# Kernel optimization log

Hardware: AMD Instinct MI355X
Metric: run time of the kernel (lower is better)

The kernel has to match this reference:

```python
import jax, jax.numpy as jnp
import numpy as np

N = 10000        # nodes
E = 320000       # edges (avg degree 32)
IN = 739         # in_channels
C = 64           # hid_channels
H = 1            # heads
D = C // H       # per-head dim
L = 10           # layer_num
G = 64           # num graphs in batch
LAMBD = 1.0


def setup_inputs() -> dict:
    key = jax.random.key(0)
    ks = jax.random.split(key, 14)
    s = 0.05
    return {
        "x": jax.random.normal(ks[0], (N, IN), jnp.float32),
        "edge_index": jax.random.randint(ks[1], (2, E), 0, N, dtype=jnp.int32),
        "batch": jnp.sort(jax.random.randint(ks[2], (N,), 0, G, dtype=jnp.int32)),
        # InitFeat: Linear(739->64), ELU, Linear(64->64) (dropout = identity at eval)
        "w0": jax.random.normal(ks[3], (IN, C), jnp.float32) * s,
        "b0": jax.random.normal(ks[4], (C,), jnp.float32) * s,
        "w1": jax.random.normal(ks[5], (C, C), jnp.float32) * s,
        "b1": jax.random.normal(ks[6], (C,), jnp.float32) * s,
        # AeroConv attention vectors for k = 1..L-1
        "conv_att": jax.random.normal(ks[7], (L - 1, H, D), jnp.float32) * s,
        # UpdateZ k=0 (g = h, width D) and k=1..L-1 (g = [h, z_scale], width 2D)
        "hop_att0": jax.random.normal(ks[8], (H, D), jnp.float32) * s,
        "hop_bias0": jax.random.normal(ks[9], (H,), jnp.float32) * s,
        "hop_att": jax.random.normal(ks[10], (L - 1, H, 2 * D), jnp.float32) * s,
        "hop_bias": jax.random.normal(ks[11], (L - 1, H), jnp.float32) * s,
        # readout head Linear(64->1)
        "w_head": jax.random.normal(ks[12], (C, 1), jnp.float32) * s,
        "b_head": jax.random.normal(ks[13], (1,), jnp.float32) * s,
    }


def reference(x, edge_index, batch, w0, b0, w1, b1, conv_att,
              hop_att0, hop_bias0, hop_att, hop_bias, w_head, b_head):
    src, dst = edge_index[0], edge_index[1]

    # ---- InitFeat (dropout is identity at inference) ----
    h = x @ w0 + b0
    h = jax.nn.elu(h) @ w1 + b1              # [N, C]
    x = h

    # ---- UpdateZ, k = 0: z = h * hop_attention ----
    hh = x.reshape(N, H, D)
    attn = jnp.sum(hop_att0 * jax.nn.elu(hh), axis=-1) + hop_bias0   # [N, H]
    z = hh * attn[..., None]                 # [N, H, D]

    for i in range(L - 1):
        k = i + 1
        scale = jnp.float32(np.log(LAMBD / k + 1.0 + 1e-6))
        z_scale = z * scale                  # [N, H, D]

        # per-edge attention: elu(z_i + z_j), dot with att, softplus
        a = jax.nn.elu(z_scale[src] + z_scale[dst])                   # [E, H, D]
        a = jax.nn.softplus(jnp.sum(conv_att[i] * a, axis=-1)) + 1e-6  # [E, H]

        # symmetric normalization by scatter-summed degree
        adj_sum = jax.ops.segment_sum(a, dst, num_segments=N)         # [N, H]
        inv = jnp.maximum(adj_sum, 1e-32) ** -0.5
        na = (inv[src] * a * inv[dst])[..., None]                     # [E, H, 1]

        # weighted scatter-sum of source features
        msgs = x[src].reshape(E, H, D) * na                           # [E, H, D]
        x = jax.ops.segment_sum(msgs, dst, num_segments=N).reshape(N, C)

        # UpdateZ (k >= 1): g = [h, z_scale]
        hh = x.reshape(N, H, D)
        g = jnp.concatenate([hh, z_scale], axis=-1)                   # [N, H, 2D]
        attn = jnp.sum(hop_att[i] * jax.nn.elu(g), axis=-1) + hop_bias[i]
        z = z + hh * attn[..., None]

    # ---- readout: elu, global mean pool over batch, linear head ----
    zf = jax.nn.elu(z.reshape(N, C))
    seg_sum = jax.ops.segment_sum(zf, batch, num_segments=G)          # [G, C]
    cnt = jax.ops.segment_sum(jnp.ones((N,), zf.dtype), batch, num_segments=G)
    pooled = seg_sum / jnp.maximum(cnt, 1.0)[:, None]
    return pooled @ w_head + b_head                                   # [G, 1]
```

## Files before the change

### kernel.cpp

```cpp
#include <hip/hip_runtime.h>
#include <hip/hip_bf16.h>
#include <math.h>

#define NN     10000
#define EE     320000
#define IN_CH  739
#define CC     64
#define GG     64
#define NLAYER 9
#define NBUCK  157
#define CHUNK  2048

typedef _Float16 half_t;
typedef _Float16 h4 __attribute__((ext_vector_type(4)));

__device__ __forceinline__ float eluf(float x) {
    return x > 0.f ? x : __expf(x) - 1.f;
}
__device__ __forceinline__ float softplusf(float x) {
    return fmaxf(x, 0.f) + __logf(1.f + __expf(-fabsf(x)));
}
__device__ __forceinline__ float wave_sum(float v) {
#pragma unroll
    for (int off = 32; off > 0; off >>= 1) v += __shfl_xor(v, off, 64);
    return v;
}
__device__ __forceinline__ float4 ldh4(const half_t* p) {
    const h4 v = *(const h4*)p;
    return make_float4((float)v.x, (float)v.y, (float)v.z, (float)v.w);
}

__global__ __launch_bounds__(256) void k_gemm1_part(
    const float* __restrict__ x, const float* __restrict__ w0,
    float* __restrict__ hpart)
{
    __shared__ float xs[64 * 68];
    __shared__ float ws[64 * 64];
    const int tid = threadIdx.x;
    const int cg = tid & 15;
    const int rg = tid >> 4;
    const int split = blockIdx.x & 3;
    const int R0 = (blockIdx.x >> 2) * 64;
    const int K0 = split * 192;

    const int sk = tid & 63;
    const int sr = tid >> 6;

    float xr[16], wr[16];
    float acc[4][4] = {};

#pragma unroll
    for (int i = 0; i < 16; ++i) {
        const int r = sr + 4 * i;
        const int gr = R0 + r;
        const int gk = K0 + sk;
        xr[i] = (gr < NN && gk < IN_CH) ? x[(size_t)gr * IN_CH + gk] : 0.f;
        const int wk = K0 + r;
        wr[i] = (wk < IN_CH) ? w0[wk * CC + sk] : 0.f;
    }

    for (int t = 0; t < 3; ++t) {
        __syncthreads();
#pragma unroll
        for (int i = 0; i < 16; ++i) {
            const int r = sr + 4 * i;
            xs[r * 68 + sk] = xr[i];
            ws[r * 64 + sk] = wr[i];
        }
        __syncthreads();
        if (t + 1 < 3) {
            const int k0 = K0 + (t + 1) * 64;
#pragma unroll
            for (int i = 0; i < 16; ++i) {
                const int r = sr + 4 * i;
                const int gr = R0 + r;
                const int gk = k0 + sk;
                xr[i] = (gr < NN && gk < IN_CH) ? x[(size_t)gr * IN_CH + gk] : 0.f;
                const int wk = k0 + r;
                wr[i] = (wk < IN_CH) ? w0[wk * CC + sk] : 0.f;
            }
        }
#pragma unroll 4
        for (int k4 = 0; k4 < 64; k4 += 4) {
            float4 xv[4], wv[4];
#pragma unroll
            for (int j = 0; j < 4; ++j)
                xv[j] = *(const float4*)&xs[(rg * 4 + j) * 68 + k4];
#pragma unroll
            for (int q = 0; q < 4; ++q)
                wv[q] = *(const float4*)&ws[(k4 + q) * 64 + cg * 4];
#pragma unroll
            for (int j = 0; j < 4; ++j) {
                const float* xf = (const float*)&xv[j];
#pragma unroll
                for (int q = 0; q < 4; ++q) {
                    const float* wf = (const float*)&wv[q];
#pragma unroll
                    for (int i = 0; i < 4; ++i)
                        acc[j][i] = fmaf(xf[q], wf[i], acc[j][i]);
                }
            }
        }
    }

#pragma unroll
    for (int j = 0; j < 4; ++j) {
        const int row = R0 + rg * 4 + j;
        if (row < NN)
            *(float4*)&hpart[((size_t)split * NN + row) * CC + cg * 4] =
                make_float4(acc[j][0], acc[j][1], acc[j][2], acc[j][3]);
    }
}

__global__ __launch_bounds__(256) void k_init2(
    const float* __restrict__ hpart,
    const float* __restrict__ b0, const float* __restrict__ w1,
    const float* __restrict__ b1,
    const float* __restrict__ hop_att0, const float* __restrict__ hop_bias0,
    float scale1,
    half_t* __restrict__ xout, float* __restrict__ zout,
    float* __restrict__ zsout, half_t* __restrict__ zshout)
{
    __shared__ float xs[32 * 68];
    __shared__ float ws[64 * 64];
    const int tid = threadIdx.x;
    const int R0 = blockIdx.x * 32;

#pragma unroll
    for (int j = 0; j < 2; ++j) {
        const int slot = tid + 256 * j;
        const int row = slot >> 4;
        const int col4 = (slot & 15) * 4;
        const int grow = R0 + row;
        float4 s = make_float4(0.f, 0.f, 0.f, 0.f);
        if (grow < NN) {
#pragma unroll
            for (int sp = 0; sp < 4; ++sp) {
                const float4 v =
                    *(const float4*)&hpart[((size_t)sp * NN + grow) * CC + col4];
                s.x += v.x; s.y += v.y; s.z += v.z; s.w += v.w;
            }
        }
        const float4 bb = *(const float4*)&b0[col4];
        s.x = eluf(s.x + bb.x); s.y = eluf(s.y + bb.y);
        s.z = eluf(s.z + bb.z); s.w = eluf(s.w + bb.w);
        *(float4*)&xs[row * 68 + col4] = s;
    }
    {
        const int sk = tid & 63;
        const int sr = tid >> 6;
#pragma unroll
        for (int i = 0; i < 16; ++i)
            ws[(sr + 4 * i) * 64 + sk] = w1[(sr + 4 * i) * CC + sk];
    }
    __syncthreads();

    const int cg = tid & 15;
    const int rg = tid >> 4;
    float acc2[2][4];
    const float4 b1v = *(const float4*)&b1[cg * 4];
#pragma unroll
    for (int j = 0; j < 2; ++j) {
        acc2[j][0] = b1v.x; acc2[j][1] = b1v.y;
        acc2[j][2] = b1v.z; acc2[j][3] = b1v.w;
    }
#pragma unroll 4
    for (int k4 = 0; k4 < 64; k4 += 4) {
        float4 xv[2], wv[4];
#pragma unroll
        for (int j = 0; j < 2; ++j)
            xv[j] = *(const float4*)&xs[(rg * 2 + j) * 68 + k4];
#pragma unroll
        for (int q = 0; q < 4; ++q)
            wv[q] = *(const float4*)&ws[(k4 + q) * 64 + cg * 4];
#pragma unroll
        for (int j = 0; j < 2; ++j) {
            const float* xf = (const float*)&xv[j];
#pragma unroll
            for (int q = 0; q < 4; ++q) {
                const float* wf = (const float*)&wv[q];
#pragma unroll
                for (int i = 0; i < 4; ++i)
                    acc2[j][i] = fmaf(xf[q], wf[i], acc2[j][i]);
            }
        }
    }

    __syncthreads();
#pragma unroll
    for (int j = 0; j < 2; ++j)
        *(float4*)&ws[(rg * 2 + j) * 64 + cg * 4] =
            make_float4(acc2[j][0], acc2[j][1], acc2[j][2], acc2[j][3]);
    __syncthreads();

    const int c = tid & 63;
    const int w = tid >> 6;
    const float ha = hop_att0[c];
    const float hb = hop_bias0[0];
#pragma unroll
    for (int rr = 0; rr < 8; ++rr) {
        const int r = w * 8 + rr;
        const float v = ws[r * 64 + c];
        const float attn = wave_sum(ha * eluf(v)) + hb;
        const int row = R0 + r;
        if (row < NN) {
            const float zv = v * attn;
            const float zs = zv * scale1;
            xout[row * CC + c] = (half_t)v;
            zout[row * CC + c] = zv;
            zsout[row * CC + c] = zs;
            zshout[row * CC + c] = (half_t)zs;
        }
    }
}

__global__ __launch_bounds__(256) void k_hist(const int* __restrict__ ei,
                                              int* __restrict__ deg)
{
    const int e = blockIdx.x * 256 + threadIdx.x;
    atomicAdd(&deg[ei[EE + e]], 1);
}

__global__ __launch_bounds__(256) void k_scan(const int* __restrict__ deg,
                                              int* __restrict__ offs,
                                              int* __restrict__ bcur)
{
    __shared__ int part[256];
    const int tid = threadIdx.x;
    const int start = tid * 40;
    const int end = start + 40 < NN ? start + 40 : NN;
    int sum = 0;
    for (int i = start; i < end; ++i) sum += deg[i];
    part[tid] = sum;
    __syncthreads();
    if (tid == 0) {
        int run = 0;
        for (int i = 0; i < 256; ++i) { int t = part[i]; part[i] = run; run += t; }
    }
    __syncthreads();
    int run = part[tid];
    for (int i = start; i < end; ++i) {
        offs[i] = run;
        if ((i & 63) == 0) bcur[i >> 6] = run;
        run += deg[i];
    }
}

__global__ __launch_bounds__(256) void k_part1(
    const int* __restrict__ ei, int* __restrict__ bcur,
    int2* __restrict__ csr_pair)
{
    __shared__ int hist[NBUCK];
    __shared__ int scan_s[NBUCK];
    __shared__ int base_g[NBUCK];
    __shared__ int lcur[NBUCK];
    __shared__ int2 staged[CHUNK];
    const int tid = threadIdx.x;
    const int e0 = blockIdx.x * CHUNK;

    for (int b = tid; b < NBUCK; b += 256) { hist[b] = 0; lcur[b] = 0; }
    __syncthreads();

    int src[8], dst[8];
#pragma unroll
    for (int j = 0; j < 8; ++j) {
        const int e = e0 + tid + 256 * j;
        if (e < EE) {
            src[j] = ei[e];
            dst[j] = ei[EE + e];
            atomicAdd(&hist[dst[j] >> 6], 1);
        } else dst[j] = -1;
    }
    __syncthreads();
    if (tid == 0) {
        int run = 0;
        for (int b = 0; b < NBUCK; ++b) { scan_s[b] = run; run += hist[b]; }
    }
    __syncthreads();
    if (tid < NBUCK && hist[tid] > 0)
        base_g[tid] = atomicAdd(&bcur[tid], hist[tid]);
    __syncthreads();
#pragma unroll
    for (int j = 0; j < 8; ++j) {
        if (dst[j] >= 0) {
            const int b = dst[j] >> 6;
            const int r = atomicAdd(&lcur[b], 1);
            staged[scan_s[b] + r] = make_int2(src[j], dst[j]);
        }
    }
    __syncthreads();
    const int tot = (EE - e0) < CHUNK ? (EE - e0) : CHUNK;
    for (int i = tid; i < tot; i += 256) {
        const int2 p = staged[i];
        const int b = p.y >> 6;
        csr_pair[base_g[b] + (i - scan_s[b])] = p;
    }
}

__global__ __launch_bounds__(256) void k_part2(
    const int* __restrict__ offs, const int2* __restrict__ csr_pair,
    int* __restrict__ csr_src)
{
    __shared__ int lcnt[64];
    __shared__ int loffs[64];
    const int b = blockIdx.x;
    const int tid = threadIdx.x;
    const int d0 = b * 64;
    if (tid < 64) {
        lcnt[tid] = 0;
        const int d = d0 + tid;
        loffs[tid] = (d < NN) ? offs[d] : EE;
    }
    __syncthreads();
    const int r0 = offs[d0];
    const int r1 = (d0 + 64 < NN) ? offs[d0 + 64] : EE;
    for (int i = r0 + tid; i < r1; i += 256) {
        const int2 p = csr_pair[i];
        const int ld = p.y & 63;
        const int r = atomicAdd(&lcnt[ld], 1);
        csr_src[loffs[ld] + r] = p.x;
    }
}

__global__ __launch_bounds__(256) void k_bounds(const int* __restrict__ batch,
                                                int* __restrict__ gstart)
{
    const int n = blockIdx.x * 256 + threadIdx.x;
    if (n >= NN) return;
    if (n == 0)
        for (int g = 0; g <= batch[0]; ++g) gstart[g] = 0;
    else {
        const int b0 = batch[n - 1], b1 = batch[n];
        for (int g = b0 + 1; g <= b1; ++g) gstart[g] = n;
    }
    if (n == NN - 1)
        for (int g = batch[NN - 1] + 1; g <= GG; ++g) gstart[g] = NN;
}

__global__ __launch_bounds__(256) void k_edge_adj(
    const int* __restrict__ offs, const int* __restrict__ deg,
    const int* __restrict__ csr_src,
    const float* __restrict__ zs_buf, const half_t* __restrict__ zsh,
    const float* __restrict__ conv_att,
    float* __restrict__ a_csr, float* __restrict__ inv_adj)
{
    const int n = blockIdx.x * 4 + (threadIdx.x >> 6);
    const int lane = threadIdx.x & 63;
    const int l = lane & 15;
    const int grp = lane >> 4;
    const int start = offs[n];
    const int len = deg[n];

    const float4 zd = *(const float4*)(zs_buf + n * CC + l * 4);
    const float4 scv = *(const float4*)(conv_att + l * 4);

    float asum = 0.f;
    int i = grp;
    for (; i + 12 < len; i += 16) {
        const int s0 = csr_src[start + i];
        const int s1 = csr_src[start + i + 4];
        const int s2 = csr_src[start + i + 8];
        const int s3 = csr_src[start + i + 12];
        const float4 a0 = ldh4(zsh + s0 * CC + l * 4);
        const float4 a1 = ldh4(zsh + s1 * CC + l * 4);
        const float4 a2 = ldh4(zsh + s2 * CC + l * 4);
        const float4 a3 = ldh4(zsh + s3 * CC + l * 4);
        float p0 = scv.x * eluf(a0.x + zd.x);
        p0 = fmaf(scv.y, eluf(a0.y + zd.y), p0);
        p0 = fmaf(scv.z, eluf(a0.z + zd.z), p0);
        p0 = fmaf(scv.w, eluf(a0.w + zd.w), p0);
        float p1 = scv.x * eluf(a1.x + zd.x);
        p1 = fmaf(scv.y, eluf(a1.y + zd.y), p1);
        p1 = fmaf(scv.z, eluf(a1.z + zd.z), p1);
        p1 = fmaf(scv.w, eluf(a1.w + zd.w), p1);
        float p2 = scv.x * eluf(a2.x + zd.x);
        p2 = fmaf(scv.y, eluf(a2.y + zd.y), p2);
        p2 = fmaf(scv.z, eluf(a2.z + zd.z), p2);
        p2 = fmaf(scv.w, eluf(a2.w + zd.w), p2);
        float p3 = scv.x * eluf(a3.x + zd.x);
        p3 = fmaf(scv.y, eluf(a3.y + zd.y), p3);
        p3 = fmaf(scv.z, eluf(a3.z + zd.z), p3);
        p3 = fmaf(scv.w, eluf(a3.w + zd.w), p3);
#pragma unroll
        for (int off = 8; off > 0; off >>= 1) {
            p0 += __shfl_xor(p0, off, 64);
            p1 += __shfl_xor(p1, off, 64);
            p2 += __shfl_xor(p2, off, 64);
            p3 += __shfl_xor(p3, off, 64);
        }
        const float ae0 = softplusf(p0) + 1e-6f;
        const float ae1 = softplusf(p1) + 1e-6f;
        const float ae2 = softplusf(p2) + 1e-6f;
        const float ae3 = softplusf(p3) + 1e-6f;
        asum += ae0 + ae1 + ae2 + ae3;
        if (l == 0) {
            a_csr[start + i] = ae0;
            a_csr[start + i + 4] = ae1;
            a_csr[start + i + 8] = ae2;
            a_csr[start + i + 12] = ae3;
        }
    }
    for (; i < len; i += 4) {
        const int s0 = csr_src[start + i];
        const float4 a0 = ldh4(zsh + s0 * CC + l * 4);
        float p0 = scv.x * eluf(a0.x + zd.x);
        p0 = fmaf(scv.y, eluf(a0.y + zd.y), p0);
        p0 = fmaf(scv.z, eluf(a0.z + zd.z), p0);
        p0 = fmaf(scv.w, eluf(a0.w + zd.w), p0);
#pragma unroll
        for (int off = 8; off > 0; off >>= 1) p0 += __shfl_xor(p0, off, 64);
        const float ae0 = softplusf(p0) + 1e-6f;
        asum += ae0;
        if (l == 0) a_csr[start + i] = ae0;
    }

    asum += __shfl_xor(asum, 16, 64);
    asum += __shfl_xor(asum, 32, 64);
    if (lane == 0) inv_adj[n] = rsqrtf(fmaxf(asum, 1e-32f));
}

__global__ __launch_bounds__(256) void k_msg_fused(
    const int* __restrict__ offs, const int* __restrict__ deg,
    const int* __restrict__ csr_src, const float* __restrict__ a_csr,
    const float* __restrict__ inv_adj, const half_t* __restrict__ x,
    half_t* __restrict__ xn, float* __restrict__ z,
    float* __restrict__ zs_buf, half_t* __restrict__ zsh,
    const float* __restrict__ hop_att, const float* __restrict__ hop_bias,
    float scale_next)
{
    const int n = blockIdx.x * 4 + (threadIdx.x >> 6);
    const int c = threadIdx.x & 63;
    const int start = offs[n];
    const int len = deg[n];
    const float invd = inv_adj[n];

    float acc = 0.f;
    for (int base = 0; base < len; base += 64) {
        const int cnt = (len - base) < 64 ? (len - base) : 64;
        int s_l = 0; float na_l = 0.f;
        if (c < cnt) {
            s_l = csr_src[start + base + c];
            na_l = a_csr[start + base + c] * inv_adj[s_l] * invd;
        }
        int j = 0;
        for (; j + 8 <= cnt; j += 8) {
            int ss[8]; float nn_[8];
#pragma unroll
            for (int q = 0; q < 8; ++q) {
                ss[q] = __builtin_amdgcn_readlane(s_l, j + q);
                nn_[q] = __int_as_float(
                    __builtin_amdgcn_readlane(__float_as_int(na_l), j + q));
            }
            float vv[8];
#pragma unroll
            for (int q = 0; q < 8; ++q) vv[q] = (float)x[ss[q] * CC + c];
#pragma unroll
            for (int q = 0; q < 8; ++q) acc = fmaf(vv[q], nn_[q], acc);
        }
        for (; j < cnt; ++j) {
            const int s = __builtin_amdgcn_readlane(s_l, j);
            const float na = __int_as_float(
                __builtin_amdgcn_readlane(__float_as_int(na_l), j));
            acc = fmaf((float)x[s * CC + c], na, acc);
        }
    }

    const float zv = z[n * CC + c];
    const float zsv = zs_buf[n * CC + c];
    float g = hop_att[c] * eluf(acc) + hop_att[CC + c] * eluf(zsv);
    const float attn = wave_sum(g) + hop_bias[0];
    const float znew = zv + acc * attn;
    const float zsnew = znew * scale_next;
    z[n * CC + c] = znew;
    zs_buf[n * CC + c] = zsnew;
    zsh[n * CC + c] = (half_t)zsnew;
    xn[n * CC + c] = (half_t)acc;
}

__global__ __launch_bounds__(256) void k_pool_head(
    const float* __restrict__ z, const int* __restrict__ gstart,
    const float* __restrict__ w_head, const float* __restrict__ b_head,
    float* __restrict__ out)
{
    __shared__ float red[4][CC];
    const int g = blockIdx.x;
    const int w = threadIdx.x >> 6;
    const int c = threadIdx.x & 63;
    const int s0 = gstart[g], s1 = gstart[g + 1];

    float acc = 0.f;
    for (int n = s0 + w; n < s1; n += 4) acc += eluf(z[n * CC + c]);
    red[w][c] = acc;
    __syncthreads();
    if (w == 0) {
        const float v = red[0][c] + red[1][c] + red[2][c] + red[3][c];
        const float tot = wave_sum(v * w_head[c]);
        if (c == 0)
            out[g] = tot / fmaxf((float)(s1 - s0), 1.f) + b_head[0];
    }
}

extern "C" void kernel_launch(void* const* d_in, const int* in_sizes, int n_in,
                              void* d_out, int out_size, void* d_ws, size_t ws_size,
                              hipStream_t stream) {
    const float* x        = (const float*)d_in[0];
    const int*   ei       = (const int*)d_in[1];
    const int*   batch    = (const int*)d_in[2];
    const float* w0       = (const float*)d_in[3];
    const float* b0       = (const float*)d_in[4];
    const float* w1       = (const float*)d_in[5];
    const float* b1       = (const float*)d_in[6];
    const float* conv_att = (const float*)d_in[7];
    const float* hop_att0 = (const float*)d_in[8];
    const float* hop_bias0= (const float*)d_in[9];
    const float* hop_att  = (const float*)d_in[10];
    const float* hop_bias = (const float*)d_in[11];
    const float* w_head   = (const float*)d_in[12];
    const float* b_head   = (const float*)d_in[13];
    float* out = (float*)d_out;

    float sc[NLAYER + 1];
    for (int k = 1; k <= NLAYER; ++k)
        sc[k] = (float)log(1.0 / (double)k + 1.0 + 1e-6);

    float* zbuf    = (float*)d_ws;
    float* zsbuf   = zbuf + NN * CC;
    float* inv_adj = zsbuf + NN * CC;
    float* hpart   = inv_adj + NN;
    float* a_csr   = hpart;
    int*   csr_src = (int*)(a_csr + EE);
    int2*  csr_pair= (int2*)(csr_src + EE);
    int*   deg     = (int*)(csr_pair + EE);
    int*   offs    = deg + NN;
    int*   bcur    = offs + NN;
    int*   gstart  = bcur + NBUCK;
    half_t* xhA = (half_t*)(hpart + 4 * NN * CC);
    half_t* xhB = xhA + NN * CC;
    half_t* zsh = xhB + NN * CC;

    k_gemm1_part<<<157 * 4, 256, 0, stream>>>(x, w0, hpart);
    k_init2<<<313, 256, 0, stream>>>(hpart, b0, w1, b1, hop_att0, hop_bias0,
                                     sc[1], xhA, zbuf, zsbuf, zsh);

    (void)hipMemsetAsync(deg, 0, (size_t)NN * 4, stream);
    k_hist<<<EE / 256, 256, 0, stream>>>(ei, deg);
    k_scan<<<1, 256, 0, stream>>>(deg, offs, bcur);
    k_part1<<<(EE + CHUNK - 1) / CHUNK, 256, 0, stream>>>(ei, bcur, csr_pair);
    k_part2<<<NBUCK, 256, 0, stream>>>(offs, csr_pair, csr_src);
    k_bounds<<<(NN + 255) / 256, 256, 0, stream>>>(batch, gstart);

    half_t* xcur = xhA;
    half_t* xnext = xhB;
    for (int i = 0; i < NLAYER; ++i) {
        const float scale_next = (i + 1 < NLAYER) ? sc[i + 2] : 0.f;
        k_edge_adj<<<NN / 4, 256, 0, stream>>>(offs, deg, csr_src, zsbuf, zsh,
                                               conv_att + i * CC,
                                               a_csr, inv_adj);
        k_msg_fused<<<NN / 4, 256, 0, stream>>>(offs, deg, csr_src, a_csr,
                                                inv_adj, xcur, xnext, zbuf,
                                                zsbuf, zsh,
                                                hop_att + i * 2 * CC,
                                                hop_bias + i, scale_next);
        half_t* t = xcur; xcur = xnext; xnext = t;
    }

    k_pool_head<<<GG, 256, 0, stream>>>(zbuf, gstart, w_head, b_head, out);
}
```

Measured before the change: 438.0 us.

## Merge setup kernels into GEMM launches and use one-wave blocks per node

The degree histogram now runs as extra blocks inside the first GEMM kernel. The scan and graph-bounds computation run as extra blocks inside the init kernel, which cuts the setup from six launches to three. The per-layer edge and message kernels change from 256-thread blocks handling four nodes to 64-thread blocks handling one node each. The workspace layout is changed so a_csr no longer aliases hpart, since the histogram now runs alongside the GEMM and a_csr needs its own space. A risk is that the scan blocks in the init kernel read deg, which depends only on the previous kernel's histogram, so it stays correct through stream ordering.

```diff
diff --git a/kernel.cpp b/kernel.cpp
--- a/kernel.cpp
+++ b/kernel.cpp
@@ -10,6 +10,7 @@
 #define NLAYER 9
 #define NBUCK  157
 #define CHUNK  2048
+#define GEMM1B 628
 
 typedef _Float16 half_t;
 typedef _Float16 h4 __attribute__((ext_vector_type(4)));
@@ -30,12 +31,20 @@
     return make_float4((float)v.x, (float)v.y, (float)v.z, (float)v.w);
 }
 
-__global__ __launch_bounds__(256) void k_gemm1_part(
+__global__ __launch_bounds__(256) void k_gemm1_hist(
     const float* __restrict__ x, const float* __restrict__ w0,
-    float* __restrict__ hpart)
+    float* __restrict__ hpart,
+    const int* __restrict__ ei, int* __restrict__ deg)
 {
     __shared__ float xs[64 * 68];
     __shared__ float ws[64 * 64];
+
+    if (blockIdx.x >= GEMM1B) {
+        const int e = (blockIdx.x - GEMM1B) * 256 + threadIdx.x;
+        atomicAdd(&deg[ei[EE + e]], 1);
+        return;
+    }
+
     const int tid = threadIdx.x;
     const int cg = tid & 15;
     const int rg = tid >> 4;
@@ -112,18 +121,57 @@
     }
 }
 
-__global__ __launch_bounds__(256) void k_init2(
+__global__ __launch_bounds__(256) void k_init2_scan(
     const float* __restrict__ hpart,
     const float* __restrict__ b0, const float* __restrict__ w1,
     const float* __restrict__ b1,
     const float* __restrict__ hop_att0, const float* __restrict__ hop_bias0,
     float scale1,
     half_t* __restrict__ xout, float* __restrict__ zout,
-    float* __restrict__ zsout, half_t* __restrict__ zshout)
+    float* __restrict__ zsout, half_t* __restrict__ zshout,
+    const int* __restrict__ deg, int* __restrict__ offs,
+    int* __restrict__ bcur,
+    const int* __restrict__ batch, int* __restrict__ gstart)
 {
     __shared__ float xs[32 * 68];
     __shared__ float ws[64 * 64];
+    __shared__ int part[256];
     const int tid = threadIdx.x;
+
+    if (blockIdx.x == 313) {
+        const int start = tid * 40;
+        const int end = start + 40 < NN ? start + 40 : NN;
+        int sum = 0;
+        for (int i = start; i < end; ++i) sum += deg[i];
+        part[tid] = sum;
+        __syncthreads();
+        if (tid == 0) {
+            int run = 0;
+            for (int i = 0; i < 256; ++i) { int t = part[i]; part[i] = run; run += t; }
+        }
+        __syncthreads();
+        int run = part[tid];
+        for (int i = start; i < end; ++i) {
+            offs[i] = run;
+            if ((i & 63) == 0) bcur[i >> 6] = run;
+            run += deg[i];
+        }
+        return;
+    }
+    if (blockIdx.x > 313) {
+        const int n = (blockIdx.x - 314) * 256 + tid;
+        if (n >= NN) return;
+        if (n == 0)
+            for (int g = 0; g <= batch[0]; ++g) gstart[g] = 0;
+        else {
+            const int b0_ = batch[n - 1], b1_ = batch[n];
+            for (int g = b0_ + 1; g <= b1_; ++g) gstart[g] = n;
+        }
+        if (n == NN - 1)
+            for (int g = batch[NN - 1] + 1; g <= GG; ++g) gstart[g] = NN;
+        return;
+    }
+
     const int R0 = blockIdx.x * 32;
 
 #pragma unroll
@@ -214,38 +262,6 @@
     }
 }
 
-__global__ __launch_bounds__(256) void k_hist(const int* __restrict__ ei,
-                                              int* __restrict__ deg)
-{
-    const int e = blockIdx.x * 256 + threadIdx.x;
-    atomicAdd(&deg[ei[EE + e]], 1);
-}
-
-__global__ __launch_bounds__(256) void k_scan(const int* __restrict__ deg,
-                                              int* __restrict__ offs,
-                                              int* __restrict__ bcur)
-{
-    __shared__ int part[256];
-    const int tid = threadIdx.x;
-    const int start = tid * 40;
-    const int end = start + 40 < NN ? start + 40 : NN;
-    int sum = 0;
-    for (int i = start; i < end; ++i) sum += deg[i];
-    part[tid] = sum;
-    __syncthreads();
-    if (tid == 0) {
-        int run = 0;
-        for (int i = 0; i < 256; ++i) { int t = part[i]; part[i] = run; run += t; }
-    }
-    __syncthreads();
-    int run = part[tid];
-    for (int i = start; i < end; ++i) {
-        offs[i] = run;
-        if ((i & 63) == 0) bcur[i >> 6] = run;
-        run += deg[i];
-    }
-}
-
 __global__ __launch_bounds__(256) void k_part1(
     const int* __restrict__ ei, int* __restrict__ bcur,
     int2* __restrict__ csr_pair)
@@ -322,30 +338,15 @@
     }
 }
 
-__global__ __launch_bounds__(256) void k_bounds(const int* __restrict__ batch,
-                                                int* __restrict__ gstart)
-{
-    const int n = blockIdx.x * 256 + threadIdx.x;
-    if (n >= NN) return;
-    if (n == 0)
-        for (int g = 0; g <= batch[0]; ++g) gstart[g] = 0;
-    else {
-        const int b0 = batch[n - 1], b1 = batch[n];
-        for (int g = b0 + 1; g <= b1; ++g) gstart[g] = n;
-    }
-    if (n == NN - 1)
-        for (int g = batch[NN - 1] + 1; g <= GG; ++g) gstart[g] = NN;
-}
-
-__global__ __launch_bounds__(256) void k_edge_adj(
+__global__ __launch_bounds__(64) void k_edge_adj(
     const int* __restrict__ offs, const int* __restrict__ deg,
     const int* __restrict__ csr_src,
     const float* __restrict__ zs_buf, const half_t* __restrict__ zsh,
     const float* __restrict__ conv_att,
     float* __restrict__ a_csr, float* __restrict__ inv_adj)
 {
-    const int n = blockIdx.x * 4 + (threadIdx.x >> 6);
-    const int lane = threadIdx.x & 63;
+    const int n = blockIdx.x;
+    const int lane = threadIdx.x;
     const int l = lane & 15;
     const int grp = lane >> 4;
     const int start = offs[n];
@@ -419,7 +420,7 @@
     if (lane == 0) inv_adj[n] = rsqrtf(fmaxf(asum, 1e-32f));
 }
 
-__global__ __launch_bounds__(256) void k_msg_fused(
+__global__ __launch_bounds__(64) void k_msg_fused(
     const int* __restrict__ offs, const int* __restrict__ deg,
     const int* __restrict__ csr_src, const float* __restrict__ a_csr,
     const float* __restrict__ inv_adj, const half_t* __restrict__ x,
@@ -428,8 +429,8 @@
     const float* __restrict__ hop_att, const float* __restrict__ hop_bias,
     float scale_next)
 {
-    const int n = blockIdx.x * 4 + (threadIdx.x >> 6);
-    const int c = threadIdx.x & 63;
+    const int n = blockIdx.x;
+    const int c = threadIdx.x;
     const int start = offs[n];
     const int len = deg[n];
     const float invd = inv_adj[n];
@@ -527,40 +528,37 @@
     float* zsbuf   = zbuf + NN * CC;
     float* inv_adj = zsbuf + NN * CC;
     float* hpart   = inv_adj + NN;
-    float* a_csr   = hpart;
+    float* a_csr   = hpart + 4 * NN * CC;
     int*   csr_src = (int*)(a_csr + EE);
     int2*  csr_pair= (int2*)(csr_src + EE);
     int*   deg     = (int*)(csr_pair + EE);
     int*   offs    = deg + NN;
     int*   bcur    = offs + NN;
     int*   gstart  = bcur + NBUCK;
-    half_t* xhA = (half_t*)(hpart + 4 * NN * CC);
+    half_t* xhA = (half_t*)(gstart + GG + 1);
     half_t* xhB = xhA + NN * CC;
     half_t* zsh = xhB + NN * CC;
 
-    k_gemm1_part<<<157 * 4, 256, 0, stream>>>(x, w0, hpart);
-    k_init2<<<313, 256, 0, stream>>>(hpart, b0, w1, b1, hop_att0, hop_bias0,
-                                     sc[1], xhA, zbuf, zsbuf, zsh);
-
     (void)hipMemsetAsync(deg, 0, (size_t)NN * 4, stream);
-    k_hist<<<EE / 256, 256, 0, stream>>>(ei, deg);
-    k_scan<<<1, 256, 0, stream>>>(deg, offs, bcur);
+    k_gemm1_hist<<<GEMM1B + EE / 256, 256, 0, stream>>>(x, w0, hpart, ei, deg);
+    k_init2_scan<<<314 + (NN + 255) / 256, 256, 0, stream>>>(
+        hpart, b0, w1, b1, hop_att0, hop_bias0, sc[1],
+        xhA, zbuf, zsbuf, zsh, deg, offs, bcur, batch, gstart);
     k_part1<<<(EE + CHUNK - 1) / CHUNK, 256, 0, stream>>>(ei, bcur, csr_pair);
     k_part2<<<NBUCK, 256, 0, stream>>>(offs, csr_pair, csr_src);
-    k_bounds<<<(NN + 255) / 256, 256, 0, stream>>>(batch, gstart);
 
     half_t* xcur = xhA;
     half_t* xnext = xhB;
     for (int i = 0; i < NLAYER; ++i) {
         const float scale_next = (i + 1 < NLAYER) ? sc[i + 2] : 0.f;
-        k_edge_adj<<<NN / 4, 256, 0, stream>>>(offs, deg, csr_src, zsbuf, zsh,
-                                               conv_att + i * CC,
-                                               a_csr, inv_adj);
-        k_msg_fused<<<NN / 4, 256, 0, stream>>>(offs, deg, csr_src, a_csr,
-                                                inv_adj, xcur, xnext, zbuf,
-                                                zsbuf, zsh,
-                                                hop_att + i * 2 * CC,
-                                                hop_bias + i, scale_next);
+        k_edge_adj<<<NN, 64, 0, stream>>>(offs, deg, csr_src, zsbuf, zsh,
+                                          conv_att + i * CC,
+                                          a_csr, inv_adj);
+        k_msg_fused<<<NN, 64, 0, stream>>>(offs, deg, csr_src, a_csr,
+                                           inv_adj, xcur, xnext, zbuf,
+                                           zsbuf, zsh,
+                                           hop_att + i * 2 * CC,
+                                           hop_bias + i, scale_next);
         half_t* t = xcur; xcur = xnext; xnext = t;
     }
 
```

Result: faster. 419.6 us (-4.2%).
